# Performance work log

Measured on AMD Instinct MI355X. Metric: run time of the kernel, lower is better.

The kernel has to match this reference:

```python
import jax, jax.numpy as jnp
import numpy as np

N, IN_DIM, HID, OUT, E = 100000, 128, 64, 40, 1600000


def setup_inputs() -> dict:
    key = jax.random.key(0)
    ks = jax.random.split(key, 10)
    x = jax.random.normal(ks[0], (N, IN_DIM), dtype=jnp.float32)
    edge_index = jax.random.randint(ks[1], (2, E), 0, N, dtype=jnp.int64)
    # GCNConv params (Glorot-ish scale)
    W1 = jax.random.normal(ks[2], (IN_DIM, HID), dtype=jnp.float32) / np.sqrt(IN_DIM)
    b1 = jnp.zeros((HID,), dtype=jnp.float32)
    W2 = jax.random.normal(ks[3], (HID, OUT), dtype=jnp.float32) / np.sqrt(HID)
    b2 = jnp.zeros((OUT,), dtype=jnp.float32)
    # KnowledgeEnhancedLayer params
    P = jax.random.normal(ks[4], (OUT,), dtype=jnp.float32)
    K = jax.random.normal(ks[5], (OUT,), dtype=jnp.float32)
    U = jax.random.normal(ks[6], (OUT,), dtype=jnp.float32)
    return {"x": x, "edge_index": edge_index, "W1": W1, "b1": b1,
            "W2": W2, "b2": b2, "P": P, "K": K, "U": U}


def reference(x, edge_index, W1, b1, W2, b2, P, K, U):
    n = x.shape[0]
    loops = jnp.arange(n, dtype=edge_index.dtype)
    src = jnp.concatenate([edge_index[0], loops])  # [E+N]
    dst = jnp.concatenate([edge_index[1], loops])
    # symmetric GCN normalization with self-loops: deg over targets
    deg = jax.ops.segment_sum(jnp.ones(dst.shape, x.dtype), dst, num_segments=n)
    dinv = jax.lax.rsqrt(deg)  # deg >= 1 due to self-loops
    norm = dinv[src] * dinv[dst]  # [E+N]

    def gcn_conv(h, W, b):
        hw = h @ W                                   # [n, out]
        msg = norm[:, None] * hw[src]                # gather + scale
        agg = jax.ops.segment_sum(msg, dst, num_segments=n)  # scatter-add
        return agg + b

    h = jax.nn.relu(gcn_conv(x, W1, b1))
    h = gcn_conv(h, W2, b2)
    y = jax.nn.relu(h + P * K * U)  # knowledge enhancement
    return jax.nn.log_softmax(y, axis=1)
```

## Files before the change

### kernel.cpp

```cpp
#include <hip/hip_runtime.h>
#include <hip/hip_bf16.h>
#include <hip/hip_fp16.h>

#define IN_DIM 128
#define HID    64
#define OUT_DIM 40
#define GRP_SH 8
#define CB_TILE 4096
#define CAP    8000

__global__ __launch_bounds__(256) void coarse_bin(const int* __restrict__ src,
                                                  const int* __restrict__ dst, int e,
                                                  int nbuk, int* __restrict__ ccur,
                                                  unsigned* __restrict__ pairs) {
    __shared__ int lcnt[512];
    __shared__ int gbase[512];
    int t = threadIdx.x;
    for (int i = t; i < nbuk; i += 256) lcnt[i] = 0;
    __syncthreads();
    int base = blockIdx.x * CB_TILE;
    int s[16], d[16];
#pragma unroll
    for (int q = 0; q < 16; ++q) {
        int i = base + q * 256 + t;
        if (i < e) { s[q] = src[i]; d[q] = dst[i]; }
        else d[q] = -1;
    }
#pragma unroll
    for (int q = 0; q < 16; ++q)
        if (d[q] >= 0) atomicAdd(&lcnt[d[q] >> GRP_SH], 1);
    __syncthreads();
    for (int b = t; b < nbuk; b += 256) {
        int c = lcnt[b];
        gbase[b] = c ? atomicAdd(&ccur[b], c) : 0;
        lcnt[b] = 0;
    }
    __syncthreads();
#pragma unroll
    for (int q = 0; q < 16; ++q) {
        if (d[q] >= 0) {
            int b = d[q] >> GRP_SH;
            int slot = gbase[b] + atomicAdd(&lcnt[b], 1);
            if (slot < CAP)
                pairs[(size_t)b * CAP + slot] =
                    ((unsigned)(d[q] & 255) << 24) | (unsigned)s[q];
        }
    }
}

__global__ void scan_coarse(const int* __restrict__ ccnt, int nbuk, int n,
                            int* __restrict__ cbase, int* __restrict__ off) {
    __shared__ int tmp[512];
    int t = threadIdx.x;
    int v = (t < nbuk) ? ccnt[t] : 0;
    tmp[t] = v;
    __syncthreads();
    for (int ofs = 1; ofs < 512; ofs <<= 1) {
        int a = (t >= ofs) ? tmp[t - ofs] : 0;
        __syncthreads();
        tmp[t] += a;
        __syncthreads();
    }
    if (t < nbuk) cbase[t] = tmp[t] - v;
    if (t == 511) { cbase[nbuk] = tmp[511]; off[n] = tmp[511]; }
}

__global__ __launch_bounds__(256) void fine_bin2(const unsigned* __restrict__ pairs,
                                                 const int* __restrict__ ccnt,
                                                 const int* __restrict__ cbase, int n,
                                                 int* __restrict__ off,
                                                 float* __restrict__ dinv,
                                                 int* __restrict__ sorted) {
    __shared__ int hist[256];
    __shared__ int lpre[256];
    int b = blockIdx.x, t = threadIdx.x;
    int nlo = b << GRP_SH;
    int nnodes = min(256, n - nlo);
    int cnt = min(ccnt[b], CAP);
    const unsigned* reg = pairs + (size_t)b * CAP;
    int gbase = cbase[b];
    hist[t] = 0;
    __syncthreads();
    for (int j = t; j < cnt; j += 256)
        atomicAdd(&hist[reg[j] >> 24], 1);
    __syncthreads();
    int v = hist[t];
    lpre[t] = v;
    __syncthreads();
    for (int ofs = 1; ofs < 256; ofs <<= 1) {
        int a = (t >= ofs) ? lpre[t - ofs] : 0;
        __syncthreads();
        lpre[t] += a;
        __syncthreads();
    }
    int goff = gbase + lpre[t] - v;
    if (t < nnodes) {
        off[nlo + t]  = goff;
        dinv[nlo + t] = rsqrtf((float)v + 1.0f);
    }
    __syncthreads();
    hist[t] = goff;
    __syncthreads();
    for (int j = t; j < cnt; j += 256) {
        unsigned p = reg[j];
        int pos = atomicAdd(&hist[p >> 24], 1);
        sorted[pos] = (int)(p & 0xFFFFFFu);
    }
}

__global__ __launch_bounds__(256) void gemm1(const float* __restrict__ x,
                                             const float* __restrict__ W1,
                                             __half* __restrict__ hw1, int n) {
    __shared__ float Ws[IN_DIM][HID];
    __shared__ float xs[32][IN_DIM];
    int tid = threadIdx.x;
    for (int i = tid * 4; i < IN_DIM * HID; i += 256 * 4)
        *(float4*)&Ws[0][i] = *(const float4*)&W1[i];
    int base = blockIdx.x * 32;
    for (int i = tid; i < 32 * IN_DIM / 4; i += 256) {
        int r = i >> 5, kk = i & 31;
        int gr = base + r;
        float4 v = {0.f, 0.f, 0.f, 0.f};
        if (gr < n) v = *(const float4*)&x[(size_t)gr * IN_DIM + kk * 4];
        *(float4*)&xs[r][kk * 4] = v;
    }
    __syncthreads();
    int col = tid & 63;
    int rg  = (tid >> 6) * 8;
    float acc[8] = {};
#pragma unroll 2
    for (int k = 0; k < IN_DIM; k += 4) {
        float w0 = Ws[k + 0][col], w1 = Ws[k + 1][col];
        float w2 = Ws[k + 2][col], w3 = Ws[k + 3][col];
#pragma unroll
        for (int r = 0; r < 8; ++r) {
            float4 xv = *(float4*)&xs[rg + r][k];
            acc[r] = fmaf(xv.x, w0, acc[r]);
            acc[r] = fmaf(xv.y, w1, acc[r]);
            acc[r] = fmaf(xv.z, w2, acc[r]);
            acc[r] = fmaf(xv.w, w3, acc[r]);
        }
    }
#pragma unroll
    for (int r = 0; r < 8; ++r) {
        int gr = base + rg + r;
        if (gr < n) hw1[(size_t)gr * HID + col] = __float2half(acc[r]);
    }
}

__global__ void gather1_h4(const __half* __restrict__ hw1, const float* __restrict__ dinv,
                           const int* __restrict__ off, const int* __restrict__ sorted,
                           const float* __restrict__ b1, __half* __restrict__ hout,
                           int n) {
    int wid  = blockIdx.x * (blockDim.x >> 6) + (threadIdx.x >> 6);
    int lane = threadIdx.x & 63;
    if (wid >= n) return;
    int g = lane >> 4;
    int c = lane & 15;
    float dd = dinv[wid];
    float4 acc = {0.f, 0.f, 0.f, 0.f};
    if (g == 0) {
        uint2 u = *(const uint2*)(hw1 + (size_t)wid * HID + 4 * c);
        __half2 h0 = *(__half2*)&u.x, h1 = *(__half2*)&u.y;
        float s2 = dd * dd;
        acc.x = s2 * __low2float(h0);  acc.y = s2 * __high2float(h0);
        acc.z = s2 * __low2float(h1);  acc.w = s2 * __high2float(h1);
    }
    int j = off[wid], en = off[wid + 1];
    for (; j + 16 <= en; j += 16) {
        int s0 = sorted[j + g],      s1 = sorted[j + 4 + g];
        int s2i = sorted[j + 8 + g], s3 = sorted[j + 12 + g];
        float w0 = dinv[s0] * dd, w1 = dinv[s1] * dd;
        float w2 = dinv[s2i] * dd, w3 = dinv[s3] * dd;
        uint2 u0 = *(const uint2*)(hw1 + (size_t)s0 * HID + 4 * c);
        uint2 u1 = *(const uint2*)(hw1 + (size_t)s1 * HID + 4 * c);
        uint2 u2 = *(const uint2*)(hw1 + (size_t)s2i * HID + 4 * c);
        uint2 u3 = *(const uint2*)(hw1 + (size_t)s3 * HID + 4 * c);
        __half2 a0 = *(__half2*)&u0.x, a1 = *(__half2*)&u0.y;
        __half2 b0 = *(__half2*)&u1.x, b1h = *(__half2*)&u1.y;
        __half2 c0 = *(__half2*)&u2.x, c1 = *(__half2*)&u2.y;
        __half2 d0 = *(__half2*)&u3.x, d1 = *(__half2*)&u3.y;
        acc.x = fmaf(w0, __low2float(a0), acc.x);
        acc.y = fmaf(w0, __high2float(a0), acc.y);
        acc.z = fmaf(w0, __low2float(a1), acc.z);
        acc.w = fmaf(w0, __high2float(a1), acc.w);
        acc.x = fmaf(w1, __low2float(b0), acc.x);
        acc.y = fmaf(w1, __high2float(b0), acc.y);
        acc.z = fmaf(w1, __low2float(b1h), acc.z);
        acc.w = fmaf(w1, __high2float(b1h), acc.w);
        acc.x = fmaf(w2, __low2float(c0), acc.x);
        acc.y = fmaf(w2, __high2float(c0), acc.y);
        acc.z = fmaf(w2, __low2float(c1), acc.z);
        acc.w = fmaf(w2, __high2float(c1), acc.w);
        acc.x = fmaf(w3, __low2float(d0), acc.x);
        acc.y = fmaf(w3, __high2float(d0), acc.y);
        acc.z = fmaf(w3, __low2float(d1), acc.z);
        acc.w = fmaf(w3, __high2float(d1), acc.w);
    }
    for (; j + 4 <= en; j += 4) {
        int s = sorted[j + g];
        float w = dinv[s] * dd;
        uint2 u = *(const uint2*)(hw1 + (size_t)s * HID + 4 * c);
        __half2 h0 = *(__half2*)&u.x, h1 = *(__half2*)&u.y;
        acc.x = fmaf(w, __low2float(h0), acc.x);
        acc.y = fmaf(w, __high2float(h0), acc.y);
        acc.z = fmaf(w, __low2float(h1), acc.z);
        acc.w = fmaf(w, __high2float(h1), acc.w);
    }
    int rem = en - j;
    if (g < rem) {
        int s = sorted[j + g];
        float w = dinv[s] * dd;
        uint2 u = *(const uint2*)(hw1 + (size_t)s * HID + 4 * c);
        __half2 h0 = *(__half2*)&u.x, h1 = *(__half2*)&u.y;
        acc.x = fmaf(w, __low2float(h0), acc.x);
        acc.y = fmaf(w, __high2float(h0), acc.y);
        acc.z = fmaf(w, __low2float(h1), acc.z);
        acc.w = fmaf(w, __high2float(h1), acc.w);
    }
    acc.x += __shfl_xor(acc.x, 16); acc.y += __shfl_xor(acc.y, 16);
    acc.z += __shfl_xor(acc.z, 16); acc.w += __shfl_xor(acc.w, 16);
    acc.x += __shfl_xor(acc.x, 32); acc.y += __shfl_xor(acc.y, 32);
    acc.z += __shfl_xor(acc.z, 32); acc.w += __shfl_xor(acc.w, 32);
    if (g == 0) {
        float4 bb = *(const float4*)&b1[4 * c];
        float rx = fmaxf(acc.x + bb.x, 0.f);
        float ry = fmaxf(acc.y + bb.y, 0.f);
        float rz = fmaxf(acc.z + bb.z, 0.f);
        float rw = fmaxf(acc.w + bb.w, 0.f);
        union { __half2 h[2]; uint2 u; } st;
        st.h[0] = __floats2half2_rn(rx, ry);
        st.h[1] = __floats2half2_rn(rz, rw);
        *(uint2*)(hout + (size_t)wid * HID + 4 * c) = st.u;
    }
}

__global__ __launch_bounds__(256) void gemm2(const __half* __restrict__ h,
                                             const float* __restrict__ W2,
                                             __half* __restrict__ hw2, int n) {
    __shared__ float Ws[HID][64];
    __shared__ float hs[32][HID];
    int tid = threadIdx.x;
    for (int i = tid; i < HID * 64; i += 256) {
        int k = i >> 6, ccol = i & 63;
        Ws[k][ccol] = (ccol < OUT_DIM) ? W2[k * OUT_DIM + ccol] : 0.f;
    }
    int base = blockIdx.x * 32;
    {
        int r  = tid >> 3;
        int k0 = (tid & 7) * 8;
        int gr = base + r;
        float4 lofl = {0,0,0,0}, hifl = {0,0,0,0};
        if (gr < n) {
            uint4 u = *(const uint4*)(h + (size_t)gr * HID + k0);
            __half2* hp = (__half2*)&u;
            lofl = make_float4(__low2float(hp[0]), __high2float(hp[0]),
                               __low2float(hp[1]), __high2float(hp[1]));
            hifl = make_float4(__low2float(hp[2]), __high2float(hp[2]),
                               __low2float(hp[3]), __high2float(hp[3]));
        }
        *(float4*)&hs[r][k0]     = lofl;
        *(float4*)&hs[r][k0 + 4] = hifl;
    }
    __syncthreads();
    int col = tid & 63;
    int rg  = (tid >> 6) * 8;
    float acc[8] = {};
#pragma unroll 2
    for (int k = 0; k < HID; k += 4) {
        float w0 = Ws[k + 0][col], w1 = Ws[k + 1][col];
        float w2 = Ws[k + 2][col], w3 = Ws[k + 3][col];
#pragma unroll
        for (int r = 0; r < 8; ++r) {
            float4 hv = *(float4*)&hs[rg + r][k];
            acc[r] = fmaf(hv.x, w0, acc[r]);
            acc[r] = fmaf(hv.y, w1, acc[r]);
            acc[r] = fmaf(hv.z, w2, acc[r]);
            acc[r] = fmaf(hv.w, w3, acc[r]);
        }
    }
    if (col < OUT_DIM) {
#pragma unroll
        for (int r = 0; r < 8; ++r) {
            int gr = base + rg + r;
            if (gr < n) hw2[(size_t)gr * OUT_DIM + col] = __float2half(acc[r]);
        }
    }
}

__global__ void gather2_fin(const __half* __restrict__ hw2, const float* __restrict__ dinv,
                            const int* __restrict__ off, const int* __restrict__ sorted,
                            const float* __restrict__ b2, const float* __restrict__ P,
                            const float* __restrict__ Kv, const float* __restrict__ U,
                            float* __restrict__ out, int n) {
    int wid  = blockIdx.x * (blockDim.x >> 6) + (threadIdx.x >> 6);
    int lane = threadIdx.x & 63;
    if (wid >= n) return;
    int g = lane / 20;
    int c = lane % 20;
    bool act = lane < 60;
    float dd = dinv[wid];
    float2 acc = {0.f, 0.f};
    if (lane < 20) {
        __half2 hv = *(const __half2*)(hw2 + (size_t)wid * OUT_DIM + 2 * c);
        acc.x = dd * dd * __low2float(hv);
        acc.y = dd * dd * __high2float(hv);
    }
    int j = off[wid], en = off[wid + 1];
    for (; j + 6 <= en; j += 6) {
        if (act) {
            int sa = sorted[j + g], sb = sorted[j + 3 + g];
            float wa = dinv[sa] * dd, wb = dinv[sb] * dd;
            __half2 va = *(const __half2*)(hw2 + (size_t)sa * OUT_DIM + 2 * c);
            __half2 vb = *(const __half2*)(hw2 + (size_t)sb * OUT_DIM + 2 * c);
            acc.x = fmaf(wa, __low2float(va), acc.x);
            acc.y = fmaf(wa, __high2float(va), acc.y);
            acc.x = fmaf(wb, __low2float(vb), acc.x);
            acc.y = fmaf(wb, __high2float(vb), acc.y);
        }
    }
    for (; j + 3 <= en; j += 3) {
        if (act) {
            int s = sorted[j + g];
            float w = dinv[s] * dd;
            __half2 v = *(const __half2*)(hw2 + (size_t)s * OUT_DIM + 2 * c);
            acc.x = fmaf(w, __low2float(v), acc.x);
            acc.y = fmaf(w, __high2float(v), acc.y);
        }
    }
    int rem = en - j;
    if (act && g < rem) {
        int s = sorted[j + g];
        float w = dinv[s] * dd;
        __half2 v = *(const __half2*)(hw2 + (size_t)s * OUT_DIM + 2 * c);
        acc.x = fmaf(w, __low2float(v), acc.x);
        acc.y = fmaf(w, __high2float(v), acc.y);
    }
    float r1x = __shfl(acc.x, lane + 20), r1y = __shfl(acc.y, lane + 20);
    float r2x = __shfl(acc.x, lane + 40), r2y = __shfl(acc.y, lane + 40);
    float vx = 0.f, vy = 0.f, mym = -INFINITY;
    if (lane < 20) {
        acc.x += r1x + r2x;
        acc.y += r1y + r2y;
        float2 bb = *(const float2*)&b2[2 * c];
        float2 pp = *(const float2*)&P[2 * c];
        float2 kk = *(const float2*)&Kv[2 * c];
        float2 uu = *(const float2*)&U[2 * c];
        vx = fmaxf(acc.x + bb.x + pp.x * kk.x * uu.x, 0.f);
        vy = fmaxf(acc.y + bb.y + pp.y * kk.y * uu.y, 0.f);
        mym = fmaxf(vx, vy);
    }
    float m = mym;
#pragma unroll
    for (int o = 16; o; o >>= 1) m = fmaxf(m, __shfl_xor(m, o));
    float ex = (lane < 20) ? __expf(vx - m) + __expf(vy - m) : 0.f;
    float ssum = ex;
#pragma unroll
    for (int o = 16; o; o >>= 1) ssum += __shfl_xor(ssum, o);
    float lse = m + __logf(ssum);
    if (lane < 20)
        *(float2*)(out + (size_t)wid * OUT_DIM + 2 * c) = make_float2(vx - lse, vy - lse);
}

extern "C" void kernel_launch(void* const* d_in, const int* in_sizes, int n_in,
                              void* d_out, int out_size, void* d_ws, size_t ws_size,
                              hipStream_t stream) {
    const float* x  = (const float*)d_in[0];
    const int*   ei = (const int*)d_in[1];
    const float* W1 = (const float*)d_in[2];
    const float* b1 = (const float*)d_in[3];
    const float* W2 = (const float*)d_in[4];
    const float* b2 = (const float*)d_in[5];
    const float* P  = (const float*)d_in[6];
    const float* K  = (const float*)d_in[7];
    const float* U  = (const float*)d_in[8];
    float* out = (float*)d_out;

    int n = in_sizes[0] / IN_DIM;
    int e = in_sizes[1] / 2;
    const int* src = ei;
    const int* dst = ei + e;

    int*      ccur   = (int*)d_ws;
    int*      cbase  = ccur + 512;
    int*      off    = cbase + 512;
    float*    dinv   = (float*)(off + n + 1);
    int*      sorted = (int*)(dinv + n);
    __half*   hw1    = (__half*)(((uintptr_t)(sorted + e) + 15) & ~(uintptr_t)15);
    __half*   h      = hw1 + (size_t)n * HID;
    __half*   hw2    = h + (size_t)n * HID;
    unsigned* pairs  = (unsigned*)hw1;

    int nbuk = (n + (1 << GRP_SH) - 1) >> GRP_SH;

    hipMemsetAsync(ccur, 0, 512 * sizeof(int), stream);
    coarse_bin<<<(e + CB_TILE - 1) / CB_TILE, 256, 0, stream>>>(src, dst, e, nbuk,
                                                                ccur, pairs);
    scan_coarse<<<1, 512, 0, stream>>>(ccur, nbuk, n, cbase, off);
    fine_bin2<<<nbuk, 256, 0, stream>>>(pairs, ccur, cbase, n, off, dinv, sorted);

    gemm1<<<(n + 31) / 32, 256, 0, stream>>>(x, W1, hw1, n);
    gather1_h4<<<(n + 3) / 4, 256, 0, stream>>>(hw1, dinv, off, sorted, b1, h, n);
    gemm2<<<(n + 31) / 32, 256, 0, stream>>>(h, W2, hw2, n);
    gather2_fin<<<(n + 3) / 4, 256, 0, stream>>>(hw2, dinv, off, sorted,
                                                 b2, P, K, U, out, n);
}
```

Baseline: 240.0 us.

## Merge coarse edge binning and first GEMM into one launch

Coarse binning of edges and the x@W1 GEMM now run as one kernel: blocks with low indices do binning and the rest do the GEMM, with their shared memory overlaid in a union. This removes a kernel launch and lets the GEMM work overlap the atomic-heavy binning. The pairs buffer is moved past hw2 so it no longer aliases hw1. This enlarges the workspace footprint and raises per-block LDS use for binning blocks to the GEMM's size, which may reduce their occupancy.

```diff
diff --git a/kernel.cpp b/kernel.cpp
--- a/kernel.cpp
+++ b/kernel.cpp
@@ -9,41 +9,80 @@
 #define CB_TILE 4096
 #define CAP    8000
 
-__global__ __launch_bounds__(256) void coarse_bin(const int* __restrict__ src,
-                                                  const int* __restrict__ dst, int e,
-                                                  int nbuk, int* __restrict__ ccur,
-                                                  unsigned* __restrict__ pairs) {
-    __shared__ int lcnt[512];
-    __shared__ int gbase[512];
+struct SMemG { float Ws[IN_DIM][HID]; float xs[32][IN_DIM]; };
+struct SMemB { int lcnt[512]; int gbase[512]; };
+union  SMemU { SMemG g; SMemB b; };
+
+__global__ __launch_bounds__(256) void bin_gemm1(
+        const int* __restrict__ src, const int* __restrict__ dst, int e,
+        int nbuk, int nbin, int* __restrict__ ccur, unsigned* __restrict__ pairs,
+        const float* __restrict__ x, const float* __restrict__ W1,
+        __half* __restrict__ hw1, int n) {
+    __shared__ SMemU sm;
     int t = threadIdx.x;
-    for (int i = t; i < nbuk; i += 256) lcnt[i] = 0;
-    __syncthreads();
-    int base = blockIdx.x * CB_TILE;
-    int s[16], d[16];
-#pragma unroll
-    for (int q = 0; q < 16; ++q) {
-        int i = base + q * 256 + t;
-        if (i < e) { s[q] = src[i]; d[q] = dst[i]; }
-        else d[q] = -1;
-    }
-#pragma unroll
-    for (int q = 0; q < 16; ++q)
-        if (d[q] >= 0) atomicAdd(&lcnt[d[q] >> GRP_SH], 1);
-    __syncthreads();
-    for (int b = t; b < nbuk; b += 256) {
-        int c = lcnt[b];
-        gbase[b] = c ? atomicAdd(&ccur[b], c) : 0;
-        lcnt[b] = 0;
-    }
-    __syncthreads();
-#pragma unroll
-    for (int q = 0; q < 16; ++q) {
-        if (d[q] >= 0) {
-            int b = d[q] >> GRP_SH;
-            int slot = gbase[b] + atomicAdd(&lcnt[b], 1);
-            if (slot < CAP)
-                pairs[(size_t)b * CAP + slot] =
-                    ((unsigned)(d[q] & 255) << 24) | (unsigned)s[q];
+    if ((int)blockIdx.x < nbin) {
+        for (int i = t; i < nbuk; i += 256) sm.b.lcnt[i] = 0;
+        __syncthreads();
+        int base = blockIdx.x * CB_TILE;
+        int s[16], d[16];
+#pragma unroll
+        for (int q = 0; q < 16; ++q) {
+            int i = base + q * 256 + t;
+            if (i < e) { s[q] = src[i]; d[q] = dst[i]; }
+            else d[q] = -1;
+        }
+#pragma unroll
+        for (int q = 0; q < 16; ++q)
+            if (d[q] >= 0) atomicAdd(&sm.b.lcnt[d[q] >> GRP_SH], 1);
+        __syncthreads();
+        for (int b = t; b < nbuk; b += 256) {
+            int c = sm.b.lcnt[b];
+            sm.b.gbase[b] = c ? atomicAdd(&ccur[b], c) : 0;
+            sm.b.lcnt[b] = 0;
+        }
+        __syncthreads();
+#pragma unroll
+        for (int q = 0; q < 16; ++q) {
+            if (d[q] >= 0) {
+                int b = d[q] >> GRP_SH;
+                int slot = sm.b.gbase[b] + atomicAdd(&sm.b.lcnt[b], 1);
+                if (slot < CAP)
+                    pairs[(size_t)b * CAP + slot] =
+                        ((unsigned)(d[q] & 255) << 24) | (unsigned)s[q];
+            }
+        }
+    } else {
+        for (int i = t * 4; i < IN_DIM * HID; i += 256 * 4)
+            *(float4*)&sm.g.Ws[0][i] = *(const float4*)&W1[i];
+        int base = (blockIdx.x - nbin) * 32;
+        for (int i = t; i < 32 * IN_DIM / 4; i += 256) {
+            int r = i >> 5, kk = i & 31;
+            int gr = base + r;
+            float4 v = {0.f, 0.f, 0.f, 0.f};
+            if (gr < n) v = *(const float4*)&x[(size_t)gr * IN_DIM + kk * 4];
+            *(float4*)&sm.g.xs[r][kk * 4] = v;
+        }
+        __syncthreads();
+        int col = t & 63;
+        int rg  = (t >> 6) * 8;
+        float acc[8] = {};
+#pragma unroll 2
+        for (int k = 0; k < IN_DIM; k += 4) {
+            float w0 = sm.g.Ws[k + 0][col], w1 = sm.g.Ws[k + 1][col];
+            float w2 = sm.g.Ws[k + 2][col], w3 = sm.g.Ws[k + 3][col];
+#pragma unroll
+            for (int r = 0; r < 8; ++r) {
+                float4 xv = *(float4*)&sm.g.xs[rg + r][k];
+                acc[r] = fmaf(xv.x, w0, acc[r]);
+                acc[r] = fmaf(xv.y, w1, acc[r]);
+                acc[r] = fmaf(xv.z, w2, acc[r]);
+                acc[r] = fmaf(xv.w, w3, acc[r]);
+            }
+        }
+#pragma unroll
+        for (int r = 0; r < 8; ++r) {
+            int gr = base + rg + r;
+            if (gr < n) hw1[(size_t)gr * HID + col] = __float2half(acc[r]);
         }
     }
 }
@@ -105,46 +144,6 @@
         unsigned p = reg[j];
         int pos = atomicAdd(&hist[p >> 24], 1);
         sorted[pos] = (int)(p & 0xFFFFFFu);
-    }
-}
-
-__global__ __launch_bounds__(256) void gemm1(const float* __restrict__ x,
-                                             const float* __restrict__ W1,
-                                             __half* __restrict__ hw1, int n) {
-    __shared__ float Ws[IN_DIM][HID];
-    __shared__ float xs[32][IN_DIM];
-    int tid = threadIdx.x;
-    for (int i = tid * 4; i < IN_DIM * HID; i += 256 * 4)
-        *(float4*)&Ws[0][i] = *(const float4*)&W1[i];
-    int base = blockIdx.x * 32;
-    for (int i = tid; i < 32 * IN_DIM / 4; i += 256) {
-        int r = i >> 5, kk = i & 31;
-        int gr = base + r;
-        float4 v = {0.f, 0.f, 0.f, 0.f};
-        if (gr < n) v = *(const float4*)&x[(size_t)gr * IN_DIM + kk * 4];
-        *(float4*)&xs[r][kk * 4] = v;
-    }
-    __syncthreads();
-    int col = tid & 63;
-    int rg  = (tid >> 6) * 8;
-    float acc[8] = {};
-#pragma unroll 2
-    for (int k = 0; k < IN_DIM; k += 4) {
-        float w0 = Ws[k + 0][col], w1 = Ws[k + 1][col];
-        float w2 = Ws[k + 2][col], w3 = Ws[k + 3][col];
-#pragma unroll
-        for (int r = 0; r < 8; ++r) {
-            float4 xv = *(float4*)&xs[rg + r][k];
-            acc[r] = fmaf(xv.x, w0, acc[r]);
-            acc[r] = fmaf(xv.y, w1, acc[r]);
-            acc[r] = fmaf(xv.z, w2, acc[r]);
-            acc[r] = fmaf(xv.w, w3, acc[r]);
-        }
-    }
-#pragma unroll
-    for (int r = 0; r < 8; ++r) {
-        int gr = base + rg + r;
-        if (gr < n) hw1[(size_t)gr * HID + col] = __float2half(acc[r]);
     }
 }
 
@@ -392,14 +391,18 @@
     unsigned* pairs  = (unsigned*)hw1;
 
     int nbuk = (n + (1 << GRP_SH) - 1) >> GRP_SH;
+    int nbin = (e + CB_TILE - 1) / CB_TILE;
+    int ngemm = (n + 31) / 32;
+
+    unsigned* pairs_safe = (unsigned*)(hw2 + (size_t)n * OUT_DIM);
+    pairs = pairs_safe;
 
     hipMemsetAsync(ccur, 0, 512 * sizeof(int), stream);
-    coarse_bin<<<(e + CB_TILE - 1) / CB_TILE, 256, 0, stream>>>(src, dst, e, nbuk,
-                                                                ccur, pairs);
+    bin_gemm1<<<nbin + ngemm, 256, 0, stream>>>(src, dst, e, nbuk, nbin, ccur, pairs,
+                                                x, W1, hw1, n);
     scan_coarse<<<1, 512, 0, stream>>>(ccur, nbuk, n, cbase, off);
     fine_bin2<<<nbuk, 256, 0, stream>>>(pairs, ccur, cbase, n, off, dinv, sorted);
 
-    gemm1<<<(n + 31) / 32, 256, 0, stream>>>(x, W1, hw1, n);
     gather1_h4<<<(n + 3) / 4, 256, 0, stream>>>(hw1, dinv, off, sorted, b1, h, n);
     gemm2<<<(n + 31) / 32, 256, 0, stream>>>(h, W2, hw2, n);
     gather2_fin<<<(n + 3) / 4, 256, 0, stream>>>(hw2, dinv, off, sorted,
```

Measured after the change: 251.4 us. 4.7% more time.
